# Performance work log

Measured on AMD Instinct MI355X. Metric: run time of the kernel, lower is better.

Reference implementation:

```python
import jax, jax.numpy as jnp
import numpy as np

IN_DIM = 256
OUT_DIM = 64
N = 8192
ALPHA = 0.2  # LeakyReLU negative slope
NEG_BIG = -9e15


def setup_inputs() -> dict:
    key = jax.random.key(0)
    k_h, k_A, k_W, k_a = jax.random.split(key, 4)
    h = jax.random.normal(k_h, (N, IN_DIM), dtype=jnp.float32)
    A = jax.random.randint(k_A, (N, N), 0, 2, dtype=jnp.int32)
    # xavier_uniform with gain=1.414
    gain = 1.414
    lim_W = gain * np.sqrt(6.0 / (IN_DIM + OUT_DIM))
    W = jax.random.uniform(k_W, (IN_DIM, OUT_DIM), minval=-lim_W, maxval=lim_W, dtype=jnp.float32)
    lim_a = gain * np.sqrt(6.0 / (2 * OUT_DIM + 1))
    a = jax.random.uniform(k_a, (2 * OUT_DIM, 1), minval=-lim_a, maxval=lim_a, dtype=jnp.float32)
    return {"h": h, "A": A, "W": W, "a": a}


def reference(h, A, W, a):
    # Wh: [N, d]
    Wh = h @ W
    # e_ij = leakyrelu([Wh_i || Wh_j] . a) = leakyrelu(Wh_i.a1 + Wh_j.a2)
    # -> avoid the O(N^2 * 2d) concat; compute rank-1 decomposition directly.
    a1 = a[:OUT_DIM, 0]   # [d]
    a2 = a[OUT_DIM:, 0]   # [d]
    f1 = Wh @ a1          # [N] contribution of source node i
    f2 = Wh @ a2          # [N] contribution of target node j
    e = jax.nn.leaky_relu(f1[:, None] + f2[None, :], negative_slope=ALPHA)  # [N, N]
    e = jnp.where(A > 0, e, NEG_BIG)
    attention = jax.nn.softmax(e, axis=1)  # [N, N]
    # dropout=0.0 (eval mode): identity
    h_prime = attention @ Wh               # [N, d]
    return jax.nn.elu(h_prime)             # concat=True -> ELU
```

## Files before the change

### kernel.cpp

```cpp
#include <hip/hip_runtime.h>
#include <math.h>
#include <stdint.h>

#define NV 8192
#define KD 256
#define DD 64
#define ALPHA 0.2f
#define TI 64
#define CJ 128
#define BLK 512

typedef _Float16 half8 __attribute__((ext_vector_type(8)));
typedef float floatx4 __attribute__((ext_vector_type(4)));

#define OFF_WHT  0
#define OFF_F1   (DD * NV / 2)
#define OFF_F2   (OFF_F1 + NV)
#define OFF_PACC (OFF_F2 + NV)

__global__ __launch_bounds__(256) void gat_pre(
    const float* __restrict__ h, const float* __restrict__ W,
    const float* __restrict__ a, ushort* __restrict__ whT,
    float* __restrict__ f1, float* __restrict__ f2) {
  __shared__ float hrow[4][KD];
  __shared__ __align__(8) ushort tw[DD][4];
  const int wv = threadIdx.x >> 6, lane = threadIdx.x & 63;
  const int i = blockIdx.x * 4 + wv;
  *(float4*)&hrow[wv][lane * 4] = *(const float4*)&h[(long long)i * KD + lane * 4];
  __syncthreads();
  float wh = 0.f;
#pragma unroll 8
  for (int c = 0; c < KD; ++c) wh += hrow[wv][c] * W[c * DD + lane];
  float p1 = wh * a[lane];
  float p2 = wh * a[DD + lane];
#pragma unroll
  for (int off = 32; off > 0; off >>= 1) {
    p1 += __shfl_down(p1, off);
    p2 += __shfl_down(p2, off);
  }
  if (lane == 0) { f1[i] = p1; f2[i] = p2; }
  union { _Float16 hf; ushort u; } cv;
  cv.hf = (_Float16)wh;
  tw[lane][wv] = cv.u;
  __syncthreads();
  if (threadIdx.x < DD) {
    *(uint2*)&whT[(long long)threadIdx.x * NV + blockIdx.x * 4] = *(uint2*)&tw[threadIdx.x][0];
  }
}

__global__ __launch_bounds__(BLK) void gat_main(
    const int* __restrict__ A, const ushort* __restrict__ whT,
    const float* __restrict__ f1, const float* __restrict__ f2,
    float* __restrict__ pacc, float* __restrict__ pl, int S) {
  __shared__ __align__(16) ushort w_lds[TI * CJ];
  __shared__ __align__(16) ushort b_lds[TI * CJ];
  __shared__ float f1_lds[TI], M_lds[TI], redf[8];

  const int tid = threadIdx.x;
  const int wave = tid >> 6, lane = tid & 63;
  const int tile = blockIdx.x & 127;
  const int s = blockIdx.x >> 7;
  const int i0 = tile * TI;
  const int jrange = NV / S;
  const int j0 = s * jrange;

  float m = -1e30f;
#pragma unroll
  for (int q = 0; q < 16; ++q) m = fmaxf(m, f2[tid + q * BLK]);
#pragma unroll
  for (int off = 32; off > 0; off >>= 1) m = fmaxf(m, __shfl_down(m, off));
  if (lane == 0) redf[wave] = m;
  __syncthreads();
  if (tid < TI) {
    float mm = redf[0];
#pragma unroll
    for (int k = 1; k < 8; ++k) mm = fmaxf(mm, redf[k]);
    float v = f1[i0 + tid];
    f1_lds[tid] = v;
    float x = v + mm;
    M_lds[tid] = x > 0.f ? x : ALPHA * x;
  }

  const int c4 = (tid & 31) * 4;
  const int k8w = (tid & 31) >> 1;
  const int sub = (tid & 1) * 8;
  const int rb = tid >> 5;
  const int mt = wave >> 1;
  const int nt0 = (wave & 1) * 2;
  const int m_ = lane & 15, quad = lane >> 4;

  floatx4 acc0 = {0.f, 0.f, 0.f, 0.f}, acc1 = {0.f, 0.f, 0.f, 0.f};
  float lp[4] = {0.f, 0.f, 0.f, 0.f};

  const int nch = jrange / CJ;
  for (int ch = 0; ch < nch; ++ch) {
    const int jb = j0 + ch * CJ;
    __syncthreads();

#pragma unroll
    for (int u = 0; u < 2; ++u) {
      const int idx = tid + u * BLK;
      const int n = idx >> 4, c = idx & 15;
      const uint4 t = *(const uint4*)(whT + (long long)n * NV + jb + 8 * (c ^ (n & 15)));
      *(uint4*)&b_lds[idx * 8] = t;
    }

    const float4 f2v = *(const float4*)(f2 + jb + c4);
#pragma unroll
    for (int p = 0; p < 4; ++p) {
      const int r = rb + 16 * p;
      const int4 a4 = *(const int4*)(A + (long long)(i0 + r) * NV + jb + c4);
      const float f1r = f1_lds[r], Mr = M_lds[r];
      float w0, w1, w2, w3;
      { float x = f1r + f2v.x; x = x > 0.f ? x : ALPHA * x; w0 = (a4.x > 0) ? __expf(x - Mr) : 0.f; }
      { float x = f1r + f2v.y; x = x > 0.f ? x : ALPHA * x; w1 = (a4.y > 0) ? __expf(x - Mr) : 0.f; }
      { float x = f1r + f2v.z; x = x > 0.f ? x : ALPHA * x; w2 = (a4.z > 0) ? __expf(x - Mr) : 0.f; }
      { float x = f1r + f2v.w; x = x > 0.f ? x : ALPHA * x; w3 = (a4.w > 0) ? __expf(x - Mr) : 0.f; }
      union { _Float16 hf[4]; uint2 u2; } pk;
      pk.hf[0] = (_Float16)w0; pk.hf[1] = (_Float16)w1;
      pk.hf[2] = (_Float16)w2; pk.hf[3] = (_Float16)w3;
      lp[p] += (float)pk.hf[0] + (float)pk.hf[1] + (float)pk.hf[2] + (float)pk.hf[3];
      *(uint2*)((char*)w_lds + (r * 16 + (k8w ^ (r & 15))) * 16 + sub) = pk.u2;
    }
    __syncthreads();

#pragma unroll
    for (int ks = 0; ks < 4; ++ks) {
      const int cc = 4 * ks + quad;
      const half8 af = *(const half8*)((const char*)w_lds + (((16 * mt + m_) * 16) + (cc ^ m_)) * 16);
      const half8 b0 = *(const half8*)((const char*)b_lds + (((16 * nt0 + m_) * 16) + (cc ^ m_)) * 16);
      const half8 b1 = *(const half8*)((const char*)b_lds + (((16 * (nt0 + 1) + m_) * 16) + (cc ^ m_)) * 16);
      acc0 = __builtin_amdgcn_mfma_f32_16x16x32_f16(af, b0, acc0, 0, 0, 0);
      acc1 = __builtin_amdgcn_mfma_f32_16x16x32_f16(af, b1, acc1, 0, 0, 0);
    }
  }

#pragma unroll
  for (int p = 0; p < 4; ++p) {
    float v = lp[p];
    v += __shfl_down(v, 16, 32);
    v += __shfl_down(v, 8, 32);
    v += __shfl_down(v, 4, 32);
    v += __shfl_down(v, 2, 32);
    v += __shfl_down(v, 1, 32);
    if ((tid & 31) == 0) pl[(long long)s * NV + i0 + rb + 16 * p] = v;
  }

#pragma unroll
  for (int reg = 0; reg < 4; ++reg) {
    const int i = i0 + 16 * mt + quad * 4 + reg;
    const long long base = ((long long)s * NV + i) * DD + m_;
    pacc[base + 16 * nt0] = acc0[reg];
    pacc[base + 16 * (nt0 + 1)] = acc1[reg];
  }
}

__global__ __launch_bounds__(256) void gat_fin(const float* __restrict__ pacc,
                                               const float* __restrict__ pl,
                                               float* __restrict__ out, int S) {
  const int idx = blockIdx.x * 256 + threadIdx.x;
  const int i = idx >> 6;
  float sum = 0.f, l = 0.f;
  for (int q = 0; q < S; ++q) sum += pacc[(long long)q * (NV * DD) + idx];
  for (int q = 0; q < S; ++q) l += pl[q * NV + i];
  const float v = sum / l;
  out[idx] = v > 0.f ? v : expm1f(v);
}

extern "C" void kernel_launch(void* const* d_in, const int* in_sizes, int n_in,
                              void* d_out, int out_size, void* d_ws, size_t ws_size,
                              hipStream_t stream) {
  const float* h = (const float*)d_in[0];
  const int* A = (const int*)d_in[1];
  const float* W = (const float*)d_in[2];
  const float* a = (const float*)d_in[3];
  float* out = (float*)d_out;
  float* ws = (float*)d_ws;

  ushort* whT = (ushort*)(ws + OFF_WHT);
  float* f1 = ws + OFF_F1;
  float* f2 = ws + OFF_F2;
  float* pacc = ws + OFF_PACC;

  int S = 4;
  while (S > 1 &&
         (size_t)(OFF_PACC + (size_t)S * (NV * DD + NV)) * sizeof(float) > ws_size)
    S >>= 1;
  float* pl = pacc + (size_t)S * NV * DD;

  gat_pre<<<NV / 4, 256, 0, stream>>>(h, W, a, whT, f1, f2);
  gat_main<<<(NV / TI) * S, BLK, 0, stream>>>(A, whT, f1, f2, pacc, pl, S);
  gat_fin<<<NV * DD / 256, 256, 0, stream>>>(pacc, pl, out, S);
}
```

Measured before the change: 395.5 us.

## Prefetch next chunk's A and Wh tiles into registers during MFMA, raise split to 8

Loads of the adjacency chunk, f2 and transposed Wh for the next j-chunk are issued into registers before the current chunk's MFMA loop, so global latency overlaps compute. f1 and the row max are hoisted into registers, explicit barriers with sched_barrier and s_setprio replace __syncthreads, and the j-split S rises from 4 to 8 for more blocks. This adds register pressure and doubles the partial-accumulator traffic in the final reduction.

```diff
diff --git a/kernel.cpp b/kernel.cpp
--- a/kernel.cpp
+++ b/kernel.cpp
@@ -80,6 +80,7 @@
     float x = v + mm;
     M_lds[tid] = x > 0.f ? x : ALPHA * x;
   }
+  __syncthreads();
 
   const int c4 = (tid & 31) * 4;
   const int k8w = (tid & 31) >> 1;
@@ -89,41 +90,76 @@
   const int nt0 = (wave & 1) * 2;
   const int m_ = lane & 15, quad = lane >> 4;
 
+  float f1r[4], Mr[4];
+#pragma unroll
+  for (int p = 0; p < 4; ++p) {
+    f1r[p] = f1_lds[rb + 16 * p];
+    Mr[p] = M_lds[rb + 16 * p];
+  }
+
   floatx4 acc0 = {0.f, 0.f, 0.f, 0.f}, acc1 = {0.f, 0.f, 0.f, 0.f};
   float lp[4] = {0.f, 0.f, 0.f, 0.f};
 
   const int nch = jrange / CJ;
-  for (int ch = 0; ch < nch; ++ch) {
-    const int jb = j0 + ch * CJ;
-    __syncthreads();
-
+
+  uint4 bw[2];
+  int4 Ar[4];
+  float4 f2v;
+  {
+    const int jb = j0;
 #pragma unroll
     for (int u = 0; u < 2; ++u) {
       const int idx = tid + u * BLK;
       const int n = idx >> 4, c = idx & 15;
-      const uint4 t = *(const uint4*)(whT + (long long)n * NV + jb + 8 * (c ^ (n & 15)));
-      *(uint4*)&b_lds[idx * 8] = t;
-    }
-
-    const float4 f2v = *(const float4*)(f2 + jb + c4);
+      bw[u] = *(const uint4*)(whT + (long long)n * NV + jb + 8 * (c ^ (n & 15)));
+    }
+    f2v = *(const float4*)(f2 + jb + c4);
+#pragma unroll
+    for (int p = 0; p < 4; ++p)
+      Ar[p] = *(const int4*)(A + (long long)(i0 + rb + 16 * p) * NV + jb + c4);
+  }
+
+  for (int ch = 0; ch < nch; ++ch) {
+#pragma unroll
+    for (int u = 0; u < 2; ++u) *(uint4*)&b_lds[(tid + u * BLK) * 8] = bw[u];
+
 #pragma unroll
     for (int p = 0; p < 4; ++p) {
       const int r = rb + 16 * p;
-      const int4 a4 = *(const int4*)(A + (long long)(i0 + r) * NV + jb + c4);
-      const float f1r = f1_lds[r], Mr = M_lds[r];
+      const int4 a4 = Ar[p];
+      const float f1p = f1r[p], Mp = Mr[p];
       float w0, w1, w2, w3;
-      { float x = f1r + f2v.x; x = x > 0.f ? x : ALPHA * x; w0 = (a4.x > 0) ? __expf(x - Mr) : 0.f; }
-      { float x = f1r + f2v.y; x = x > 0.f ? x : ALPHA * x; w1 = (a4.y > 0) ? __expf(x - Mr) : 0.f; }
-      { float x = f1r + f2v.z; x = x > 0.f ? x : ALPHA * x; w2 = (a4.z > 0) ? __expf(x - Mr) : 0.f; }
-      { float x = f1r + f2v.w; x = x > 0.f ? x : ALPHA * x; w3 = (a4.w > 0) ? __expf(x - Mr) : 0.f; }
+      { float x = f1p + f2v.x; x = x > 0.f ? x : ALPHA * x; w0 = (a4.x > 0) ? __expf(x - Mp) : 0.f; }
+      { float x = f1p + f2v.y; x = x > 0.f ? x : ALPHA * x; w1 = (a4.y > 0) ? __expf(x - Mp) : 0.f; }
+      { float x = f1p + f2v.z; x = x > 0.f ? x : ALPHA * x; w2 = (a4.z > 0) ? __expf(x - Mp) : 0.f; }
+      { float x = f1p + f2v.w; x = x > 0.f ? x : ALPHA * x; w3 = (a4.w > 0) ? __expf(x - Mp) : 0.f; }
       union { _Float16 hf[4]; uint2 u2; } pk;
       pk.hf[0] = (_Float16)w0; pk.hf[1] = (_Float16)w1;
       pk.hf[2] = (_Float16)w2; pk.hf[3] = (_Float16)w3;
       lp[p] += (float)pk.hf[0] + (float)pk.hf[1] + (float)pk.hf[2] + (float)pk.hf[3];
       *(uint2*)((char*)w_lds + (r * 16 + (k8w ^ (r & 15))) * 16 + sub) = pk.u2;
     }
-    __syncthreads();
-
+
+    if (ch + 1 < nch) {
+      const int jb = j0 + (ch + 1) * CJ;
+#pragma unroll
+      for (int u = 0; u < 2; ++u) {
+        const int idx = tid + u * BLK;
+        const int n = idx >> 4, c = idx & 15;
+        bw[u] = *(const uint4*)(whT + (long long)n * NV + jb + 8 * (c ^ (n & 15)));
+      }
+      f2v = *(const float4*)(f2 + jb + c4);
+#pragma unroll
+      for (int p = 0; p < 4; ++p)
+        Ar[p] = *(const int4*)(A + (long long)(i0 + rb + 16 * p) * NV + jb + c4);
+    }
+
+    asm volatile("s_waitcnt lgkmcnt(0)" ::: "memory");
+    __builtin_amdgcn_sched_barrier(0);
+    __builtin_amdgcn_s_barrier();
+    __builtin_amdgcn_sched_barrier(0);
+
+    __builtin_amdgcn_s_setprio(1);
 #pragma unroll
     for (int ks = 0; ks < 4; ++ks) {
       const int cc = 4 * ks + quad;
@@ -133,6 +169,12 @@
       acc0 = __builtin_amdgcn_mfma_f32_16x16x32_f16(af, b0, acc0, 0, 0, 0);
       acc1 = __builtin_amdgcn_mfma_f32_16x16x32_f16(af, b1, acc1, 0, 0, 0);
     }
+    __builtin_amdgcn_s_setprio(0);
+
+    asm volatile("s_waitcnt lgkmcnt(0)" ::: "memory");
+    __builtin_amdgcn_sched_barrier(0);
+    __builtin_amdgcn_s_barrier();
+    __builtin_amdgcn_sched_barrier(0);
   }
 
 #pragma unroll
@@ -182,7 +224,7 @@
   float* f2 = ws + OFF_F2;
   float* pacc = ws + OFF_PACC;
 
-  int S = 4;
+  int S = 8;
   while (S > 1 &&
          (size_t)(OFF_PACC + (size_t)S * (NV * DD + NV)) * sizeof(float) > ws_size)
     S >>= 1;
```

New measurement: 414.1 us. 1.05x slower.
